# Performance work log

Measured on AMD Instinct MI355X. Metric: run time of the kernel, lower is better.

The kernel has to match this reference:

```python
import jax, jax.numpy as jnp
import numpy as np

H = 768        # bert hidden_size
HID = 512      # lstm_hidden
HALF = HID // 2
T = 20         # tagset_size
START, STOP = 18, 19
S = 16386      # input positions incl. CLS/SEP
NEG = -10000.0


def setup_inputs() -> dict:
    key = jax.random.key(0)
    ks = jax.random.split(key, 12)
    sc_x = 1.0
    x = jax.random.normal(ks[0], (1, S, H), dtype=jnp.float32)
    # PyTorch LSTM params (gate order i,f,g,o), one layer, bidirectional
    s_ih = 1.0 / np.sqrt(HALF)
    w_ih_f = jax.random.uniform(ks[1], (4 * HALF, H), jnp.float32, -s_ih, s_ih)
    w_hh_f = jax.random.uniform(ks[2], (4 * HALF, HALF), jnp.float32, -s_ih, s_ih)
    b_ih_f = jax.random.uniform(ks[3], (4 * HALF,), jnp.float32, -s_ih, s_ih)
    b_hh_f = jax.random.uniform(ks[4], (4 * HALF,), jnp.float32, -s_ih, s_ih)
    w_ih_b = jax.random.uniform(ks[5], (4 * HALF, H), jnp.float32, -s_ih, s_ih)
    w_hh_b = jax.random.uniform(ks[6], (4 * HALF, HALF), jnp.float32, -s_ih, s_ih)
    b_ih_b = jax.random.uniform(ks[7], (4 * HALF,), jnp.float32, -s_ih, s_ih)
    b_hh_b = jax.random.uniform(ks[8], (4 * HALF,), jnp.float32, -s_ih, s_ih)
    s_t = 1.0 / np.sqrt(HID)
    w_tag = jax.random.uniform(ks[9], (T, HID), jnp.float32, -s_t, s_t)
    b_tag = jax.random.uniform(ks[10], (T,), jnp.float32, -s_t, s_t)
    transitions = jax.random.normal(ks[11], (T, T), dtype=jnp.float32)
    transitions = transitions.at[START, :].set(NEG).at[:, STOP].set(NEG)
    return {
        "x": x,
        "w_ih_f": w_ih_f, "w_hh_f": w_hh_f, "b_ih_f": b_ih_f, "b_hh_f": b_hh_f,
        "w_ih_b": w_ih_b, "w_hh_b": w_hh_b, "b_ih_b": b_ih_b, "b_hh_b": b_hh_b,
        "w_tag": w_tag, "b_tag": b_tag, "transitions": transitions,
    }


def _lstm_one_step(xt, w_ih, b_ih, b_hh):
    # Original passes [1, N, H] to a batch_first=False LSTM => seq_len=1,
    # batch=N, zero initial state. So each token does ONE cell step:
    # h0=c0=0 => hh contribution is only b_hh.
    g = xt @ w_ih.T + b_ih + b_hh          # [N, 4*HALF]
    i, f, gg, o = jnp.split(g, 4, axis=-1)  # PyTorch gate order i,f,g,o
    c = jax.nn.sigmoid(i) * jnp.tanh(gg)    # f*c0 = 0
    return jax.nn.sigmoid(o) * jnp.tanh(c)  # [N, HALF]


def reference(x, w_ih_f, w_hh_f, b_ih_f, b_hh_f,
              w_ih_b, w_hh_b, b_ih_b, b_hh_b,
              w_tag, b_tag, transitions):
    tok = x[0, 1:-1, :]                     # narrow(1,1,S-2): drop CLS/SEP -> [N,H]
    h_f = _lstm_one_step(tok, w_ih_f, b_ih_f, b_hh_f)
    h_b = _lstm_one_step(tok, w_ih_b, b_ih_b, b_hh_b)
    enc = jnp.concatenate([h_f, h_b], axis=-1)   # [N, HID]
    feats = enc @ w_tag.T + b_tag                # [N, T] emission scores

    # ---- Viterbi decode (sequential DP over tokens) ----
    init = jnp.full((T,), NEG, dtype=feats.dtype).at[START].set(0.0)

    def vstep(fv, feat):
        scores = fv[None, :] + transitions       # [next_tag, prev_tag]
        bp = jnp.argmax(scores, axis=1)          # backpointers [T]
        fv_new = jnp.max(scores, axis=1) + feat
        return fv_new, bp

    fv, bps = jax.lax.scan(vstep, init, feats)   # bps: [N, T]
    terminal = fv + transitions[STOP]
    best = jnp.argmax(terminal)
    path_score = terminal[best]

    def btrack(b, bp):
        return bp[b], b                          # emit tag at time t, move to t-1

    _, best_path = jax.lax.scan(btrack, best, bps, reverse=True)  # [N] in time order
    return path_score, best_path
```

## Files before the change

kernel.cpp:

```cpp
#include <hip/hip_runtime.h>
#include <math.h>

#define HDIM 768
#define HIDD 512
#define NTOK 16384
#define NT 20
#define CHUNKS 128
#define CLEN 128

typedef unsigned short ushort_t;
typedef __attribute__((ext_vector_type(8))) short bf16x8;
typedef __attribute__((ext_vector_type(4))) float f32x4;

__device__ __forceinline__ float sigm(float x){ return 1.0f/(1.0f+expf(-x)); }

__device__ __forceinline__ ushort_t f2bf(float f){
    unsigned int u = __float_as_uint(f);
    unsigned int r = (u + 0x7fffu + ((u >> 16) & 1u)) >> 16;
    return (ushort_t)r;
}
__device__ __forceinline__ float bf2f(ushort_t b){
    return __uint_as_float(((unsigned int)b) << 16);
}

#define GLD16(gp, lp) __builtin_amdgcn_global_load_lds( \
    (const __attribute__((address_space(1))) void*)(gp), \
    (__attribute__((address_space(3))) void*)(lp), 16, 0, 0)

union U8 { ushort_t u[8]; uint4 v; };

__global__ __launch_bounds__(256) void conv_kernel(
    const float* __restrict__ wf, const float* __restrict__ wb,
    ushort_t* __restrict__ Bh, ushort_t* __restrict__ Bl)
{
    int t = blockIdx.x*256 + threadIdx.x;
    int n = t / 192, c4 = (t - n*192)*4;
    int dir = n / 768, nr = n - dir*768;
    int gate = nr >> 8, j = nr & 255;
    int wrow = j + ((gate==0)?0:((gate==1)?512:768));
    const float* src = dir ? wb : wf;
    const float4 v = *(const float4*)(src + (size_t)wrow*HDIM + c4);
    float f[4] = {v.x, v.y, v.z, v.w};
    ushort_t h[4], l[4];
    #pragma unroll
    for (int i=0;i<4;++i){
        h[i] = f2bf(f[i]);
        l[i] = f2bf(f[i] - bf2f(h[i]));
    }
    *(ushort4*)(Bh + (size_t)n*HDIM + c4) = make_ushort4(h[0],h[1],h[2],h[3]);
    *(ushort4*)(Bl + (size_t)n*HDIM + c4) = make_ushort4(l[0],l[1],l[2],l[3]);
}

__global__ __launch_bounds__(256, 2) void gemm_fused(
    const float* __restrict__ x,
    const ushort_t* __restrict__ Bh, const ushort_t* __restrict__ Bl,
    const float* __restrict__ bihf, const float* __restrict__ bhhf,
    const float* __restrict__ bihb, const float* __restrict__ bhhb,
    const float* __restrict__ wtag, float* __restrict__ featsp)
{
    __shared__ __align__(16) char smem[57344];
    ushort_t* As_h = (ushort_t*)smem;
    ushort_t* As_l = (ushort_t*)(smem + 4096);
    float* hbuf = (float*)smem;
    float* wts  = (float*)(smem + 8448);

    const int tid = threadIdx.x;
    const int bx = blockIdx.x;
    const int xcd = bx & 7, bidx = bx >> 3;
    const int q = bidx & 7, mt = (bidx >> 3)*8 + xcd;
    const int dir = q >> 2, j0 = (q & 3)*64;
    const int row0 = mt*64;
    const float* __restrict__ bih = dir ? bihb : bihf;
    const float* __restrict__ bhh = dir ? bhhb : bhhf;

    const int lane = tid & 63, wv = tid >> 6;
    const int wm = wv >> 1, wn = wv & 1;
    const int lm = lane & 15, lq = lane >> 4;
    const int wbB = (tid & 192) * 16;

    const int P_ = tid >> 3, s_ = tid & 7;
    const int q_ = s_ ^ (P_ & 7);
    const int mA = (P_ << 1) | (q_ >> 2);
    const int k8s = q_ & 3;
    const float* aSrc = x + (size_t)(row0 + mA + 1)*HDIM + k8s*8;
    size_t bOff[3];
    #pragma unroll
    for (int g=0; g<3; ++g)
        bOff[g] = (size_t)(dir*768 + g*256 + j0 + mA)*HDIM + k8s*8;

    int aoffB[2], boffB[2];
    #pragma unroll
    for (int f=0; f<2; ++f){
        int m = wm*32 + f*16 + lm;
        aoffB[f] = ((m>>1)*8 + ((((m&1)<<2)|lq) ^ ((m>>1)&7)))*16;
        int n = wn*32 + f*16 + lm;
        boffB[f] = ((n>>1)*8 + ((((n&1)<<2)|lq) ^ ((n>>1)&7)))*16;
    }

    int jcol[2];
    #pragma unroll
    for (int f=0; f<2; ++f) jcol[f] = j0 + wn*32 + f*16 + lm;

    f32x4 acc[3][2][2];
    #pragma unroll
    for (int g=0; g<3; ++g)
        #pragma unroll
        for (int fm=0; fm<2; ++fm)
            #pragma unroll
            for (int fn=0; fn<2; ++fn)
                acc[g][fm][fn] = (f32x4){0.f,0.f,0.f,0.f};

    uint4 rh, rl;

    {
        char* bb = smem + 8192;
        #pragma unroll
        for (int g=0; g<3; ++g){
            GLD16(Bh + bOff[g], bb + g*8192 + wbB);
            GLD16(Bl + bOff[g], bb + g*8192 + 4096 + wbB);
        }
        float4 ra0 = *(const float4*)(aSrc);
        float4 ra1 = *(const float4*)(aSrc + 4);
        float f[8] = {ra0.x,ra0.y,ra0.z,ra0.w,ra1.x,ra1.y,ra1.z,ra1.w};
        U8 h8, l8;
        #pragma unroll
        for (int i=0;i<8;++i){
            ushort_t h = f2bf(f[i]);
            h8.u[i] = h; l8.u[i] = f2bf(f[i] - bf2f(h));
        }
        rh = h8.v; rl = l8.v;
    }

    #pragma unroll 1
    for (int kt=0; kt<24; ++kt){
        __syncthreads();
        *(uint4*)&As_h[tid*8] = rh;
        *(uint4*)&As_l[tid*8] = rl;
        __syncthreads();

        if (kt < 23){
            const int k0n = (kt+1)*32;
            char* bb = smem + 8192 + ((kt+1)&1)*24576;
            #pragma unroll
            for (int g=0; g<3; ++g){
                GLD16(Bh + bOff[g] + k0n, bb + g*8192 + wbB);
                GLD16(Bl + bOff[g] + k0n, bb + g*8192 + 4096 + wbB);
            }
            float4 ra0 = *(const float4*)(aSrc + k0n);
            float4 ra1 = *(const float4*)(aSrc + k0n + 4);
            float f[8] = {ra0.x,ra0.y,ra0.z,ra0.w,ra1.x,ra1.y,ra1.z,ra1.w};
            U8 h8, l8;
            #pragma unroll
            for (int i=0;i<8;++i){
                ushort_t h = f2bf(f[i]);
                h8.u[i] = h; l8.u[i] = f2bf(f[i] - bf2f(h));
            }
            rh = h8.v; rl = l8.v;
        }

        const char* bb = smem + 8192 + (kt&1)*24576;
        bf16x8 afh[2], afl[2];
        #pragma unroll
        for (int f=0; f<2; ++f){
            afh[f] = *(const bf16x8*)(smem + aoffB[f]);
            afl[f] = *(const bf16x8*)(smem + 4096 + aoffB[f]);
        }
        #pragma unroll
        for (int g=0; g<3; ++g){
            const char* bg = bb + g*8192;
            #pragma unroll
            for (int fn=0; fn<2; ++fn){
                bf16x8 bh = *(const bf16x8*)(bg + boffB[fn]);
                bf16x8 bl = *(const bf16x8*)(bg + 4096 + boffB[fn]);
                #pragma unroll
                for (int fm=0; fm<2; ++fm){
                    acc[g][fm][fn] = __builtin_amdgcn_mfma_f32_16x16x32_bf16(
                        afh[fm], bh, acc[g][fm][fn], 0, 0, 0);
                    acc[g][fm][fn] = __builtin_amdgcn_mfma_f32_16x16x32_bf16(
                        afl[fm], bh, acc[g][fm][fn], 0, 0, 0);
                    acc[g][fm][fn] = __builtin_amdgcn_mfma_f32_16x16x32_bf16(
                        afh[fm], bl, acc[g][fm][fn], 0, 0, 0);
                }
            }
        }
    }

    float bi[2], bg_[2], bo[2];
    #pragma unroll
    for (int f=0; f<2; ++f){
        bi[f]  = bih[jcol[f]]       + bhh[jcol[f]];
        bg_[f] = bih[512 + jcol[f]] + bhh[512 + jcol[f]];
        bo[f]  = bih[768 + jcol[f]] + bhh[768 + jcol[f]];
    }
    float hv[2][2][4];
    #pragma unroll
    for (int fm=0; fm<2; ++fm)
        #pragma unroll
        for (int fn=0; fn<2; ++fn)
            #pragma unroll
            for (int r=0; r<4; ++r){
                float cv = sigm(acc[0][fm][fn][r] + bi[fn]) *
                           tanhf(acc[1][fm][fn][r] + bg_[fn]);
                hv[fm][fn][r] = sigm(acc[2][fm][fn][r] + bo[fn]) * tanhf(cv);
            }

    __syncthreads();
    for (int i2=tid; i2<NT*64; i2+=256){
        int t = i2 >> 6, j = i2 & 63;
        wts[i2] = wtag[t*HIDD + dir*256 + j0 + j];
    }
    float* fq = featsp + (size_t)q * (NTOK*NT);
    #pragma unroll 1
    for (int ph=0; ph<2; ++ph){
        __syncthreads();
        if (wm == ph){
            #pragma unroll
            for (int fm=0; fm<2; ++fm)
                #pragma unroll
                for (int fn=0; fn<2; ++fn)
                    #pragma unroll
                    for (int r=0; r<4; ++r){
                        int mloc = fm*16 + lq*4 + r;
                        int jloc = wn*32 + fn*16 + lm;
                        hbuf[mloc*65 + jloc] = hv[fm][fn][r];
                    }
        }
        __syncthreads();
        const int mrow = tid & 31, grp = tid >> 5;
        if (grp < 5){
            const int tg0 = grp*4;
            float s[4] = {0.f,0.f,0.f,0.f};
            for (int j=0;j<64;++j){
                float h = hbuf[mrow*65 + j];
                #pragma unroll
                for (int tt=0; tt<4; ++tt)
                    s[tt] = fmaf(h, wts[(tg0+tt)*64 + j], s[tt]);
            }
            const int mglob = row0 + ph*32 + mrow;
            #pragma unroll
            for (int tt=0; tt<4; ++tt)
                fq[(size_t)mglob*NT + tg0 + tt] = s[tt];
        }
    }
}

__device__ __forceinline__ void load_fl(
    const float* __restrict__ featsp, const float* __restrict__ btg,
    float* fl, int c, int tid, int nthr)
{
    const int base = c*(CLEN*NT/4);
    for (int idx=tid; idx<CLEN*NT/4; idx+=nthr){
        float4 s[8];
        #pragma unroll
        for (int p=0; p<8; ++p)
            s[p] = ((const float4*)(featsp + (size_t)p*NTOK*NT))[base+idx];
        float4 v;
        v.x = ((s[0].x+s[1].x)+(s[2].x+s[3].x)) + ((s[4].x+s[5].x)+(s[6].x+s[7].x));
        v.y = ((s[0].y+s[1].y)+(s[2].y+s[3].y)) + ((s[4].y+s[5].y)+(s[6].y+s[7].y));
        v.z = ((s[0].z+s[1].z)+(s[2].z+s[3].z)) + ((s[4].z+s[5].z)+(s[6].z+s[7].z));
        v.w = ((s[0].w+s[1].w)+(s[2].w+s[3].w)) + ((s[4].w+s[5].w)+(s[6].w+s[7].w));
        int t0 = (idx*4) % 20;
        v.x += btg[t0]; v.y += btg[t0+1]; v.z += btg[t0+2]; v.w += btg[t0+3];
        ((float4*)fl)[idx] = v;
    }
}

__global__ __launch_bounds__(512) void vit_chunkmat(
    const float* __restrict__ featsp, const float* __restrict__ btag,
    const float* __restrict__ trans, float* __restrict__ Pall)
{
    __shared__ float fl[CLEN*NT];
    __shared__ float Pb[2][NT*NT];
    const int c = blockIdx.x, tid = threadIdx.x;
    load_fl(featsp, btag, fl, c, tid, 512);
    const bool act = tid < NT*NT;
    const int i = tid/20, j = tid - i*20;
    float tr[NT];
    if (act){
        #pragma unroll
        for (int k=0;k<NT;++k) tr[k] = trans[i*NT+k];
        Pb[0][tid] = (i==j) ? 0.f : -1e30f;
    }
    __syncthreads();
    int cur = 0;
    for (int t=0;t<CLEN;++t){
        float m = -3.0e38f;
        if (act){
            #pragma unroll
            for (int k=0;k<NT;++k) m = fmaxf(m, tr[k] + Pb[cur][k*NT+j]);
            m += fl[t*NT+i];
            Pb[cur^1][tid] = m;
        }
        __syncthreads();
        cur ^= 1;
    }
    if (act) Pall[(size_t)c*(NT*NT) + tid] = Pb[cur][tid];
}

__global__ __launch_bounds__(128) void vit_replay(
    const float* __restrict__ featsp, const float* __restrict__ btag,
    const float* __restrict__ trans, const float* __restrict__ Pall,
    unsigned int* __restrict__ bpout, int* __restrict__ Hout,
    float* __restrict__ dout, int* __restrict__ bestws)
{
    __shared__ float fl[CLEN*NT];
    __shared__ float fv[NT];
    __shared__ float Pb[NT*NT];
    __shared__ unsigned char bp[CLEN*NT];
    const int c = blockIdx.x, tid = threadIdx.x;
    load_fl(featsp, btag, fl, c, tid, 128);
    if (tid<NT) fv[tid] = (tid==18) ? 0.f : -10000.f;
    float4 pn = {0.f,0.f,0.f,0.f};
    if (tid<100 && c>0) pn = ((const float4*)Pall)[tid];
    __syncthreads();
    for (int cc=0; cc<c; ++cc){
        if (tid<100) ((float4*)Pb)[tid] = pn;
        if (tid<100 && cc+1<c) pn = ((const float4*)(Pall + (size_t)(cc+1)*(NT*NT)))[tid];
        __syncthreads();
        float nf = -3.0e38f;
        if (tid<NT){
            #pragma unroll
            for (int j=0;j<NT;++j) nf = fmaxf(nf, Pb[tid*NT+j] + fv[j]);
        }
        __syncthreads();
        if (tid<NT) fv[tid] = nf;
        __syncthreads();
    }
    float tr[NT];
    if (tid<NT){
        #pragma unroll
        for (int k=0;k<NT;++k) tr[k] = trans[tid*NT+k];
    }
    __syncthreads();
    for (int t=0;t<CLEN;++t){
        float best = 0.f; int bj = 0;
        if (tid<NT){
            best = tr[0] + fv[0];
            #pragma unroll
            for (int j=1;j<NT;++j){
                float v = tr[j] + fv[j];
                if (v > best){ best = v; bj = j; }
            }
        }
        __syncthreads();
        if (tid<NT){
            fv[tid] = best + fl[t*NT+tid];
            bp[t*NT+tid] = (unsigned char)bj;
        }
        __syncthreads();
    }
    for (int idx=tid; idx<CLEN*NT/4; idx+=128)
        bpout[(size_t)c*(CLEN*NT/4) + idx] = ((unsigned int*)bp)[idx];
    if (tid<NT){
        int m = tid;
        for (int t=CLEN-1;t>=0;--t) m = bp[t*NT+m];
        Hout[c*NT+tid] = m;
    }
    if (c == CHUNKS-1 && tid == 0){
        float best = -3.0e38f; int bidx = 0;
        for (int j=0;j<NT;++j){
            float tv = fv[j] + trans[19*NT+j];
            if (tv > best){ best = tv; bidx = j; }
        }
        dout[0] = best;
        bestws[0] = bidx;
    }
}

__global__ __launch_bounds__(64) void bt_fill(
    const unsigned int* __restrict__ bpin, const int* __restrict__ Hin,
    const int* __restrict__ bestws, float* __restrict__ dout)
{
    __shared__ int Hl[CHUNKS*NT];
    __shared__ unsigned char bp[CLEN*NT];
    __shared__ float ob[CLEN];
    const int c = blockIdx.x, tid = threadIdx.x;
    for (int idx=tid; idx<CHUNKS*NT; idx+=64) Hl[idx] = Hin[idx];
    for (int idx=tid; idx<CLEN*NT/4; idx+=64)
        ((unsigned int*)bp)[idx] = bpin[(size_t)c*(CLEN*NT/4) + idx];
    __syncthreads();
    if (tid==0){
        int e = bestws[0];
        for (int cc=CHUNKS-1; cc>c; --cc) e = Hl[cc*NT+e];
        for (int t=CLEN-1;t>=0;--t){ ob[t] = (float)e; e = bp[t*NT+e]; }
    }
    __syncthreads();
    for (int idx=tid; idx<CLEN; idx+=64)
        dout[1 + c*CLEN + idx] = ob[idx];
}

extern "C" void kernel_launch(void* const* d_in, const int* in_sizes, int n_in,
                              void* d_out, int out_size, void* d_ws, size_t ws_size,
                              hipStream_t stream)
{
    const float* x    = (const float*)d_in[0];
    const float* wf   = (const float*)d_in[1];
    const float* bihf = (const float*)d_in[3];
    const float* bhhf = (const float*)d_in[4];
    const float* wb   = (const float*)d_in[5];
    const float* bihb = (const float*)d_in[7];
    const float* bhhb = (const float*)d_in[8];
    const float* wtag = (const float*)d_in[9];
    const float* btag = (const float*)d_in[10];
    const float* trans= (const float*)d_in[11];
    float* out = (float*)d_out;

    char* w = (char*)d_ws;
    ushort_t* Bh = (ushort_t*)w;         w += 2359296;
    ushort_t* Bl = (ushort_t*)w;         w += 2359296;
    float* featsp = (float*)w;           w += 10485760;
    float* Pall  = (float*)w;            w += 204800;
    int* Hmap    = (int*)w;              w += 10240;
    unsigned int* bp = (unsigned int*)w; w += 327680;
    int* best    = (int*)w;

    conv_kernel<<<1152, 256, 0, stream>>>(wf, wb, Bh, Bl);
    gemm_fused<<<2048, 256, 0, stream>>>(x, Bh, Bl, bihf, bhhf, bihb, bhhb,
                                         wtag, featsp);
    vit_chunkmat<<<CHUNKS, 512, 0, stream>>>(featsp, btag, trans, Pall);
    vit_replay<<<CHUNKS, 128, 0, stream>>>(featsp, btag, trans, Pall, bp, Hmap,
                                           out, best);
    bt_fill<<<CHUNKS, 64, 0, stream>>>(bp, Hmap, best, out);
}
```

Before: 393.9 us.

## Pre-split activations to bf16 hi/lo and stream A tiles via async LDS loads

The conversion kernel now also splits the token activations into bf16 high and low halves in workspace. The GEMM then loads A tiles with global_load_lds into a double-buffered shared-memory region, the same way it already loads B. This removes the per-k-step register staging, the in-loop conversion and one barrier. The cost is an extra full pass that reads the activations and writes the two bf16 copies, about 50 MB of extra writes, plus a larger LDS footprint.

Result: no change. 391.7 us (-0.5%).

```diff
diff --git a/kernel.cpp b/kernel.cpp
--- a/kernel.cpp
+++ b/kernel.cpp
@@ -27,40 +27,54 @@
     (const __attribute__((address_space(1))) void*)(gp), \
     (__attribute__((address_space(3))) void*)(lp), 16, 0, 0)
 
-union U8 { ushort_t u[8]; uint4 v; };
-
 __global__ __launch_bounds__(256) void conv_kernel(
+    const float* __restrict__ x,
     const float* __restrict__ wf, const float* __restrict__ wb,
+    ushort_t* __restrict__ Ah, ushort_t* __restrict__ Al,
     ushort_t* __restrict__ Bh, ushort_t* __restrict__ Bl)
 {
-    int t = blockIdx.x*256 + threadIdx.x;
-    int n = t / 192, c4 = (t - n*192)*4;
-    int dir = n / 768, nr = n - dir*768;
-    int gate = nr >> 8, j = nr & 255;
-    int wrow = j + ((gate==0)?0:((gate==1)?512:768));
-    const float* src = dir ? wb : wf;
-    const float4 v = *(const float4*)(src + (size_t)wrow*HDIM + c4);
-    float f[4] = {v.x, v.y, v.z, v.w};
-    ushort_t h[4], l[4];
-    #pragma unroll
-    for (int i=0;i<4;++i){
-        h[i] = f2bf(f[i]);
-        l[i] = f2bf(f[i] - bf2f(h[i]));
-    }
-    *(ushort4*)(Bh + (size_t)n*HDIM + c4) = make_ushort4(h[0],h[1],h[2],h[3]);
-    *(ushort4*)(Bl + (size_t)n*HDIM + c4) = make_ushort4(l[0],l[1],l[2],l[3]);
+    const int bid = blockIdx.x;
+    if (bid < 1152){
+        int t = bid*256 + threadIdx.x;
+        int n = t / 192, c4 = (t - n*192)*4;
+        int dir = n / 768, nr = n - dir*768;
+        int gate = nr >> 8, j = nr & 255;
+        int wrow = j + ((gate==0)?0:((gate==1)?512:768));
+        const float* src = dir ? wb : wf;
+        const float4 v = *(const float4*)(src + (size_t)wrow*HDIM + c4);
+        float f[4] = {v.x, v.y, v.z, v.w};
+        ushort_t h[4], l[4];
+        #pragma unroll
+        for (int i=0;i<4;++i){
+            h[i] = f2bf(f[i]);
+            l[i] = f2bf(f[i] - bf2f(h[i]));
+        }
+        *(ushort4*)(Bh + (size_t)n*HDIM + c4) = make_ushort4(h[0],h[1],h[2],h[3]);
+        *(ushort4*)(Bl + (size_t)n*HDIM + c4) = make_ushort4(l[0],l[1],l[2],l[3]);
+    } else {
+        int t = (bid-1152)*256 + threadIdx.x;
+        int row = t / 192, c4 = (t - row*192)*4;
+        const float4 v = *(const float4*)(x + (size_t)(row+1)*HDIM + c4);
+        float f[4] = {v.x, v.y, v.z, v.w};
+        ushort_t h[4], l[4];
+        #pragma unroll
+        for (int i=0;i<4;++i){
+            h[i] = f2bf(f[i]);
+            l[i] = f2bf(f[i] - bf2f(h[i]));
+        }
+        *(ushort4*)(Ah + (size_t)row*HDIM + c4) = make_ushort4(h[0],h[1],h[2],h[3]);
+        *(ushort4*)(Al + (size_t)row*HDIM + c4) = make_ushort4(l[0],l[1],l[2],l[3]);
+    }
 }
 
 __global__ __launch_bounds__(256, 2) void gemm_fused(
-    const float* __restrict__ x,
+    const ushort_t* __restrict__ Ah, const ushort_t* __restrict__ Al,
     const ushort_t* __restrict__ Bh, const ushort_t* __restrict__ Bl,
     const float* __restrict__ bihf, const float* __restrict__ bhhf,
     const float* __restrict__ bihb, const float* __restrict__ bhhb,
     const float* __restrict__ wtag, float* __restrict__ featsp)
 {
-    __shared__ __align__(16) char smem[57344];
-    ushort_t* As_h = (ushort_t*)smem;
-    ushort_t* As_l = (ushort_t*)(smem + 4096);
+    __shared__ __align__(16) char smem[65536];
     float* hbuf = (float*)smem;
     float* wts  = (float*)(smem + 8448);
 
@@ -82,7 +96,7 @@
     const int q_ = s_ ^ (P_ & 7);
     const int mA = (P_ << 1) | (q_ >> 2);
     const int k8s = q_ & 3;
-    const float* aSrc = x + (size_t)(row0 + mA + 1)*HDIM + k8s*8;
+    const size_t aoff = (size_t)(row0 + mA)*HDIM + k8s*8;
     size_t bOff[3];
     #pragma unroll
     for (int g=0; g<3; ++g)
@@ -110,60 +124,41 @@
             for (int fn=0; fn<2; ++fn)
                 acc[g][fm][fn] = (f32x4){0.f,0.f,0.f,0.f};
 
-    uint4 rh, rl;
-
     {
-        char* bb = smem + 8192;
+        GLD16(Ah + aoff, smem + wbB);
+        GLD16(Al + aoff, smem + 4096 + wbB);
+        char* bb = smem + 16384;
         #pragma unroll
         for (int g=0; g<3; ++g){
             GLD16(Bh + bOff[g], bb + g*8192 + wbB);
             GLD16(Bl + bOff[g], bb + g*8192 + 4096 + wbB);
         }
-        float4 ra0 = *(const float4*)(aSrc);
-        float4 ra1 = *(const float4*)(aSrc + 4);
-        float f[8] = {ra0.x,ra0.y,ra0.z,ra0.w,ra1.x,ra1.y,ra1.z,ra1.w};
-        U8 h8, l8;
-        #pragma unroll
-        for (int i=0;i<8;++i){
-            ushort_t h = f2bf(f[i]);
-            h8.u[i] = h; l8.u[i] = f2bf(f[i] - bf2f(h));
-        }
-        rh = h8.v; rl = l8.v;
     }
 
     #pragma unroll 1
     for (int kt=0; kt<24; ++kt){
         __syncthreads();
-        *(uint4*)&As_h[tid*8] = rh;
-        *(uint4*)&As_l[tid*8] = rl;
-        __syncthreads();
 
         if (kt < 23){
             const int k0n = (kt+1)*32;
-            char* bb = smem + 8192 + ((kt+1)&1)*24576;
+            char* ab = smem + ((kt+1)&1)*8192;
+            char* bb = smem + 16384 + ((kt+1)&1)*24576;
+            GLD16(Ah + aoff + k0n, ab + wbB);
+            GLD16(Al + aoff + k0n, ab + 4096 + wbB);
             #pragma unroll
             for (int g=0; g<3; ++g){
                 GLD16(Bh + bOff[g] + k0n, bb + g*8192 + wbB);
                 GLD16(Bl + bOff[g] + k0n, bb + g*8192 + 4096 + wbB);
             }
-            float4 ra0 = *(const float4*)(aSrc + k0n);
-            float4 ra1 = *(const float4*)(aSrc + k0n + 4);
-            float f[8] = {ra0.x,ra0.y,ra0.z,ra0.w,ra1.x,ra1.y,ra1.z,ra1.w};
-            U8 h8, l8;
-            #pragma unroll
-            for (int i=0;i<8;++i){
-                ushort_t h = f2bf(f[i]);
-                h8.u[i] = h; l8.u[i] = f2bf(f[i] - bf2f(h));
-            }
-            rh = h8.v; rl = l8.v;
-        }
-
-        const char* bb = smem + 8192 + (kt&1)*24576;
+        }
+
+        const char* ab = smem + (kt&1)*8192;
+        const char* bb = smem + 16384 + (kt&1)*24576;
         bf16x8 afh[2], afl[2];
         #pragma unroll
         for (int f=0; f<2; ++f){
-            afh[f] = *(const bf16x8*)(smem + aoffB[f]);
-            afl[f] = *(const bf16x8*)(smem + 4096 + aoffB[f]);
+            afh[f] = *(const bf16x8*)(ab + aoffB[f]);
+            afl[f] = *(const bf16x8*)(ab + 4096 + aoffB[f]);
         }
         #pragma unroll
         for (int g=0; g<3; ++g){
@@ -406,6 +401,8 @@
     float* out = (float*)d_out;
 
     char* w = (char*)d_ws;
+    ushort_t* Ah = (ushort_t*)w;         w += 25165824;
+    ushort_t* Al = (ushort_t*)w;         w += 25165824;
     ushort_t* Bh = (ushort_t*)w;         w += 2359296;
     ushort_t* Bl = (ushort_t*)w;         w += 2359296;
     float* featsp = (float*)w;           w += 10485760;
@@ -414,8 +411,8 @@
     unsigned int* bp = (unsigned int*)w; w += 327680;
     int* best    = (int*)w;
 
-    conv_kernel<<<1152, 256, 0, stream>>>(wf, wb, Bh, Bl);
-    gemm_fused<<<2048, 256, 0, stream>>>(x, Bh, Bl, bihf, bhhf, bihb, bhhb,
+    conv_kernel<<<13440, 256, 0, stream>>>(x, wf, wb, Ah, Al, Bh, Bl);
+    gemm_fused<<<2048, 256, 0, stream>>>(Ah, Al, Bh, Bl, bihf, bhhf, bihb, bhhb,
                                          wtag, featsp);
     vit_chunkmat<<<CHUNKS, 512, 0, stream>>>(featsp, btag, trans, Pall);
     vit_replay<<<CHUNKS, 128, 0, stream>>>(featsp, btag, trans, Pall, bp, Hmap,
```
